# Kernel tuning notes

Measured on AMD Instinct MI355X. Metric: run time of the kernel, lower is better.

The kernel has to match this reference:

```python
import jax, jax.numpy as jnp
import numpy as np

EPS = 1e-6
NEG_SLOPE = 0.2


def setup_inputs() -> dict:
    key = jax.random.key(0)
    k1, k2 = jax.random.split(key)
    B, D, T = 4, 512, 2048
    H, Dh = 8, 512 // 8
    x = jax.random.normal(k1, (B, D, T), dtype=jnp.float32)
    qkv = jax.random.normal(k2, (3, H, D, Dh), dtype=jnp.float32) * 0.02
    norm_w = jnp.ones((1,), dtype=jnp.float32)
    return {"x": x, "qkv": qkv, "norm_w": norm_w}


def reference(x, qkv, norm_w):
    B, D, T = x.shape
    H = qkv.shape[1]
    # leaky relu on channels-first input
    x = jnp.where(x >= 0, x, NEG_SLOPE * x)
    # fused QKV projection: (B,D,T),(3,H,D,Dh) -> (3,B,H,T,Dh)
    h = jnp.einsum('bdt,nhdD->nbhtD', x, qkv)
    # RMSNorm over the sequence axis (dim=-2), scalar learned weight
    denom = jnp.mean(h * h, axis=-2, keepdims=True)
    h = norm_w * (h / jnp.sqrt(denom + EPS))
    q, k, v = h[0], h[1], h[2]
    scale = jnp.sqrt(jnp.asarray(D // H, dtype=x.dtype))
    # manual attention: (B,H,T,T) score matrix
    attn = jax.nn.softmax(jnp.einsum('bhtD,bhTD->bhtT', q, k) / scale, axis=-1)
    # weighted values, output laid out (B,H,Dh,T) then merged to (B,D,T)
    out = jnp.einsum('bhtT,bhTD->bhDt', attn, v)
    return out.reshape(B, D, T)
```

## Files before the change

### kernel.cpp

```cpp
#include <hip/hip_runtime.h>
#include <cstddef>

#define B   4
#define D   512
#define T   2048
#define H   8
#define DH  64
#define NEG_SLOPE 0.2f
#define EPS 1e-6f
#define LOG2E 1.44269504088896340736f

typedef __attribute__((ext_vector_type(8))) short short8;
typedef __attribute__((ext_vector_type(4))) short sh4;
typedef __attribute__((ext_vector_type(4))) float float4v;

__device__ __forceinline__ float bf2f(ushort u) {
    unsigned int x = ((unsigned int)u) << 16;
    return __builtin_bit_cast(float, x);
}
__device__ __forceinline__ ushort f2bf(float f) {
    unsigned int x = __builtin_bit_cast(unsigned int, f);
    x = x + 0x7fffu + ((x >> 16) & 1u);
    return (ushort)(x >> 16);
}

__global__ __launch_bounds__(256) void transpose_fused(const float* __restrict__ x,
                                                       const float* __restrict__ qkv,
                                                       ushort* __restrict__ xT,
                                                       ushort* __restrict__ WT,
                                                       float* __restrict__ ssq, int zcount) {
    const int tid = threadIdx.x;
    const int z = blockIdx.z;
    if (z == 0 && blockIdx.x == 0 && blockIdx.y == 0) {
        for (int i = tid; i < zcount; i += 256) ssq[i] = 0.f;
    }

    const float* s;
    ushort* d;
    int src_ld, dst_ld, do_lrelu;
    if (z < B) {
        const int c0 = blockIdx.x * 64, r0 = blockIdx.y * 64;
        s = x + (size_t)z * D * T + (size_t)r0 * T + c0;
        d = xT + (size_t)z * T * D + (size_t)c0 * D + r0;
        src_ld = T; dst_ld = D; do_lrelu = 1;
    } else {
        if (blockIdx.x != 0) return;
        const int g = z - B;
        const int r0 = blockIdx.y * 64;
        s = qkv + (size_t)g * D * DH + (size_t)r0 * DH;
        d = WT + (size_t)g * DH * D + r0;
        src_ld = DH; dst_ld = D; do_lrelu = 0;
    }

    __shared__ float Ls[64][68];
    const int rl = tid >> 4, c4 = (tid & 15) * 4;
    #pragma unroll
    for (int p = 0; p < 4; ++p) {
        float4 v = *(const float4*)(s + (size_t)(rl + p * 16) * src_ld + c4);
        if (do_lrelu) {
            v.x = fmaxf(v.x, NEG_SLOPE * v.x);
            v.y = fmaxf(v.y, NEG_SLOPE * v.y);
            v.z = fmaxf(v.z, NEG_SLOPE * v.z);
            v.w = fmaxf(v.w, NEG_SLOPE * v.w);
        }
        *(float4*)&Ls[rl + p * 16][c4] = v;
    }
    __syncthreads();

    const int tl = tid >> 2;
    #pragma unroll
    for (int it = 0; it < 2; ++it) {
        int ch = (tid & 3) + it * 4;
        ushort o[8];
        #pragma unroll
        for (int j = 0; j < 8; ++j) o[j] = f2bf(Ls[ch * 8 + j][tl]);
        *(uint4*)(d + (size_t)tl * dst_ld + ch * 8) = *(uint4*)o;
    }
}

__global__ __launch_bounds__(256) void qkv_mm(const ushort* __restrict__ xT,
                                              const ushort* __restrict__ WT,
                                              ushort* __restrict__ hb,
                                              ushort* __restrict__ vT,
                                              float* __restrict__ ssq) {
    const int tid = threadIdx.x, wave = tid >> 6, lane = tid & 63;
    const int quad = lane >> 4, l16 = lane & 15;
    const int wr = wave >> 1, wc = wave & 1;
    const int t0  = blockIdx.x * 128;
    const int gd0 = blockIdx.y * 128;
    const int b   = blockIdx.z;

    __shared__ ushort SMEM[2 * 128 * 64];
    ushort* At = SMEM;
    ushort* Bt = SMEM + 128 * 64;

    const ushort* xb = xT + (size_t)b * T * D + (size_t)t0 * D;
    const ushort* wb = WT + (size_t)gd0 * D;

    const int srow = lane >> 3;
    const int csrc = (lane & 7) ^ srow;
    const bool is_v = (blockIdx.y >= 8);
    const ushort* Asrc = is_v ? At : Bt;
    const ushort* Bsrc = is_v ? Bt : At;
    const int arow0 = is_v ? wr * 64 : wc * 64;
    const int brow0 = is_v ? wc * 64 : wr * 64;

    float4v acc[4][4];
    #pragma unroll
    for (int i = 0; i < 4; ++i)
        #pragma unroll
        for (int j = 0; j < 4; ++j) acc[i][j] = (float4v){0.f, 0.f, 0.f, 0.f};

    for (int k0 = 0; k0 < D; k0 += 64) {
        #pragma unroll
        for (int i = 0; i < 4; ++i) {
            int rbase = wave * 32 + i * 8;
            int row = rbase + srow;
            __builtin_amdgcn_global_load_lds(
                (const __attribute__((address_space(1))) unsigned int*)(xb + (size_t)row * D + k0 + csrc * 8),
                (__attribute__((address_space(3))) unsigned int*)&At[rbase * 64], 16, 0, 0);
            __builtin_amdgcn_global_load_lds(
                (const __attribute__((address_space(1))) unsigned int*)(wb + (size_t)row * D + k0 + csrc * 8),
                (__attribute__((address_space(3))) unsigned int*)&Bt[rbase * 64], 16, 0, 0);
        }
        __syncthreads();

        #pragma unroll
        for (int kh = 0; kh < 2; ++kh) {
            short8 aF[4], bF[4];
            #pragma unroll
            for (int mt = 0; mt < 4; ++mt) {
                int row = arow0 + mt * 16 + l16;
                aF[mt] = *(const short8*)&Asrc[row * 64 + (((kh * 4 + quad) ^ (l16 & 7)) * 8)];
            }
            #pragma unroll
            for (int nt = 0; nt < 4; ++nt) {
                int row = brow0 + nt * 16 + l16;
                bF[nt] = *(const short8*)&Bsrc[row * 64 + (((kh * 4 + quad) ^ (l16 & 7)) * 8)];
            }
            #pragma unroll
            for (int mt = 0; mt < 4; ++mt)
                #pragma unroll
                for (int nt = 0; nt < 4; ++nt)
                    acc[mt][nt] = __builtin_amdgcn_mfma_f32_16x16x32_bf16(
                        aF[mt], bF[nt], acc[mt][nt], 0, 0, 0);
        }
        __syncthreads();
    }

    const int g  = blockIdx.y * 2 + wc;
    const int n  = g >> 3, hh = g & 7;
    const int ch = ((n * B + b) * H + hh) * 64;
    ushort* E = SMEM + wave * 4096;

    #pragma unroll
    for (int mt = 0; mt < 4; ++mt) {
        #pragma unroll
        for (int nt = 0; nt < 4; ++nt) {
            float4v c = acc[mt][nt];
            ushort4 pk;
            pk.x = f2bf(c[0]); pk.y = f2bf(c[1]);
            pk.z = f2bf(c[2]); pk.w = f2bf(c[3]);
            int row   = nt * 16 + l16;
            int chunk = mt * 2 + (quad >> 1);
            int pos   = chunk ^ (l16 & 7);
            *(ushort4*)&E[row * 64 + pos * 8 + (quad & 1) * 4] = pk;
        }
    }

    const int rsub = lane >> 3;
    const int csub = lane & 7;
    const int posr = csub ^ rsub;

    if (!is_v) {
        ushort* hbase = hb + (((size_t)n * B + b) * H + hh) * (size_t)T * DH
                        + (size_t)(t0 + wr * 64) * DH;
        float sq8[8] = {0.f, 0.f, 0.f, 0.f, 0.f, 0.f, 0.f, 0.f};
        #pragma unroll
        for (int i = 0; i < 8; ++i) {
            uint4 v = *(const uint4*)&E[(i * 8 + rsub) * 64 + posr * 8];
            const ushort* u = (const ushort*)&v;
            #pragma unroll
            for (int j = 0; j < 8; ++j) { float f = bf2f(u[j]); sq8[j] += f * f; }
            *(uint4*)(hbase + (size_t)(i * 8 + rsub) * DH + csub * 8) = v;
        }
        #pragma unroll
        for (int j = 0; j < 8; ++j) {
            float s = sq8[j];
            s += __shfl_xor(s, 8); s += __shfl_xor(s, 16); s += __shfl_xor(s, 32);
            if (lane < 8) atomicAdd(&ssq[ch + lane * 8 + j], s);
        }
    } else {
        ushort* vbase = vT + ((size_t)b * H + hh) * (size_t)DH * T + (t0 + wr * 64);
        #pragma unroll
        for (int i = 0; i < 8; ++i) {
            uint4 v = *(const uint4*)&E[(i * 8 + rsub) * 64 + posr * 8];
            const ushort* u = (const ushort*)&v;
            float s = 0.f;
            #pragma unroll
            for (int j = 0; j < 8; ++j) { float f = bf2f(u[j]); s += f * f; }
            *(uint4*)(vbase + (size_t)(i * 8 + rsub) * T + csub * 8) = v;
            s += __shfl_xor(s, 1); s += __shfl_xor(s, 2); s += __shfl_xor(s, 4);
            if ((lane & 7) == 0) atomicAdd(&ssq[ch + i * 8 + rsub], s);
        }
    }
}

__global__ __launch_bounds__(256) void flash_attn(const ushort* __restrict__ hb,
                                                  const ushort* __restrict__ vT,
                                                  const float* __restrict__ ssq,
                                                  const float* __restrict__ norm_w,
                                                  float* __restrict__ out) {
    const int tid  = threadIdx.x;
    const int wave = tid >> 6;
    const int lane = tid & 63;
    const int quad = lane >> 4;
    const int l16  = lane & 15;

    const int lin  = blockIdx.x;
    const int head = ((lin & 7) << 2) | ((lin >> 3) & 3);
    const int t0   = (lin >> 5) * 128;
    const int b    = head >> 3, hh = head & 7;

    const size_t slab = (size_t)B * H * T * DH;
    const ushort* qp = hb + (size_t)head * T * DH;
    const ushort* kp = hb + slab + (size_t)head * T * DH;
    const ushort* vp = vT + (size_t)head * DH * T;

    __shared__ ushort Kt[2][64 * 64];
    __shared__ ushort Vt[2][64 * 64];
    __shared__ float fqk[64], sv[64];

    if (tid < 64) {
        float nw = norm_w[0];
        float mq = ssq[(0 * B * H + head) * 64 + tid] * (1.0f / T) + EPS;
        float mk = ssq[(1 * B * H + head) * 64 + tid] * (1.0f / T) + EPS;
        float mv = ssq[(2 * B * H + head) * 64 + tid] * (1.0f / T) + EPS;
        fqk[tid] = nw * nw * rsqrtf(mq) * rsqrtf(mk) * 0.125f * LOG2E;
        sv[tid]  = nw * rsqrtf(mv);
    }
    __syncthreads();

    short8 bQ[2][2];
    #pragma unroll
    for (int qg = 0; qg < 2; ++qg) {
        const ushort* qr = qp + (size_t)(t0 + wave * 32 + qg * 16 + l16) * DH;
        #pragma unroll
        for (int kh = 0; kh < 2; ++kh) {
            short8 raw = *(const short8*)(qr + kh * 32 + quad * 8);
            #pragma unroll
            for (int j = 0; j < 8; ++j) {
                float f = bf2f((ushort)raw[j]) * fqk[kh * 32 + quad * 8 + j];
                bQ[qg][kh][j] = (short)f2bf(f);
            }
        }
    }

    const int srow = lane >> 3;
    const int csrc = (lane & 7) ^ srow;
    const ushort* kA = kp + (size_t)(wave * 16 + srow) * DH + csrc * 8;
    const ushort* kB = kp + (size_t)(wave * 16 + 8 + srow) * DH + csrc * 8;
    const ushort* vA = vp + (size_t)(wave * 16 + srow) * T + csrc * 8;
    const ushort* vB = vp + (size_t)(wave * 16 + 8 + srow) * T + csrc * 8;

    float l_run[2] = {0.f, 0.f};
    float4v O[2][4];
    #pragma unroll
    for (int qg = 0; qg < 2; ++qg)
        #pragma unroll
        for (int dt = 0; dt < 4; ++dt) O[qg][dt] = (float4v){0.f, 0.f, 0.f, 0.f};

    __builtin_amdgcn_global_load_lds(
        (const __attribute__((address_space(1))) unsigned int*)kA,
        (__attribute__((address_space(3))) unsigned int*)&Kt[0][(wave * 16) * 64], 16, 0, 0);
    __builtin_amdgcn_global_load_lds(
        (const __attribute__((address_space(1))) unsigned int*)kB,
        (__attribute__((address_space(3))) unsigned int*)&Kt[0][(wave * 16 + 8) * 64], 16, 0, 0);
    __builtin_amdgcn_global_load_lds(
        (const __attribute__((address_space(1))) unsigned int*)vA,
        (__attribute__((address_space(3))) unsigned int*)&Vt[0][(wave * 16) * 64], 16, 0, 0);
    __builtin_amdgcn_global_load_lds(
        (const __attribute__((address_space(1))) unsigned int*)vB,
        (__attribute__((address_space(3))) unsigned int*)&Vt[0][(wave * 16 + 8) * 64], 16, 0, 0);

    for (int jt = 0; jt < 32; ++jt) {
        __syncthreads();
        if (jt < 31) {
            const int pn = (jt + 1) & 1;
            const size_t jk = (size_t)(jt + 1) * 64;
            __builtin_amdgcn_global_load_lds(
                (const __attribute__((address_space(1))) unsigned int*)(kA + jk * DH),
                (__attribute__((address_space(3))) unsigned int*)&Kt[pn][(wave * 16) * 64], 16, 0, 0);
            __builtin_amdgcn_global_load_lds(
                (const __attribute__((address_space(1))) unsigned int*)(kB + jk * DH),
                (__attribute__((address_space(3))) unsigned int*)&Kt[pn][(wave * 16 + 8) * 64], 16, 0, 0);
            __builtin_amdgcn_global_load_lds(
                (const __attribute__((address_space(1))) unsigned int*)(vA + jk),
                (__attribute__((address_space(3))) unsigned int*)&Vt[pn][(wave * 16) * 64], 16, 0, 0);
            __builtin_amdgcn_global_load_lds(
                (const __attribute__((address_space(1))) unsigned int*)(vB + jk),
                (__attribute__((address_space(3))) unsigned int*)&Vt[pn][(wave * 16 + 8) * 64], 16, 0, 0);
        }
        const int p = jt & 1;

        float4v S[2][4];
        #pragma unroll
        for (int qg = 0; qg < 2; ++qg)
            #pragma unroll
            for (int mt = 0; mt < 4; ++mt) S[qg][mt] = (float4v){0.f, 0.f, 0.f, 0.f};
        #pragma unroll
        for (int kh = 0; kh < 2; ++kh) {
            #pragma unroll
            for (int mt = 0; mt < 4; ++mt) {
                int row = mt * 16 + l16;
                short8 aK = *(const short8*)&Kt[p][row * 64 + (((kh * 4 + quad) ^ (row & 7)) * 8)];
                #pragma unroll
                for (int qg = 0; qg < 2; ++qg)
                    S[qg][mt] = __builtin_amdgcn_mfma_f32_16x16x32_bf16(aK, bQ[qg][kh], S[qg][mt], 0, 0, 0);
            }
        }

        sh4 bP[2][4];
        #pragma unroll
        for (int qg = 0; qg < 2; ++qg) {
            #pragma unroll
            for (int mt = 0; mt < 4; ++mt) {
                float p0 = __builtin_amdgcn_exp2f(S[qg][mt][0]);
                float p1 = __builtin_amdgcn_exp2f(S[qg][mt][1]);
                float p2 = __builtin_amdgcn_exp2f(S[qg][mt][2]);
                float p3 = __builtin_amdgcn_exp2f(S[qg][mt][3]);
                l_run[qg] += (p0 + p1) + (p2 + p3);
                unsigned int a0 = __builtin_bit_cast(unsigned int, p0) + 0x8000u;
                unsigned int a1 = __builtin_bit_cast(unsigned int, p1) + 0x8000u;
                unsigned int a2 = __builtin_bit_cast(unsigned int, p2) + 0x8000u;
                unsigned int a3 = __builtin_bit_cast(unsigned int, p3) + 0x8000u;
                uint2 pk;
                pk.x = __builtin_amdgcn_perm(a1, a0, 0x07060302u);
                pk.y = __builtin_amdgcn_perm(a3, a2, 0x07060302u);
                bP[qg][mt] = __builtin_bit_cast(sh4, pk);
            }
        }

        #pragma unroll
        for (int mt = 0; mt < 4; ++mt) {
            #pragma unroll
            for (int dt = 0; dt < 4; ++dt) {
                int dd = dt * 16 + l16;
                sh4 aV = *(const sh4*)&Vt[p][dd * 64 + (((mt * 2 + (quad >> 1)) ^ (dd & 7)) * 8)
                                            + (quad & 1) * 4];
                #pragma unroll
                for (int qg = 0; qg < 2; ++qg)
                    O[qg][dt] = __builtin_amdgcn_mfma_f32_16x16x16bf16_1k(
                        aV, bP[qg][mt], O[qg][dt], 0, 0, 0);
            }
        }
    }

    #pragma unroll
    for (int qg = 0; qg < 2; ++qg) {
        float rs = l_run[qg];
        rs += __shfl_xor(rs, 16);
        rs += __shfl_xor(rs, 32);
        float inv = 1.f / rs;
        const int t = t0 + wave * 32 + qg * 16 + l16;
        #pragma unroll
        for (int dt = 0; dt < 4; ++dt) {
            #pragma unroll
            for (int r = 0; r < 4; ++r) {
                int dd = dt * 16 + quad * 4 + r;
                out[((size_t)b * D + hh * DH + dd) * T + t] = O[qg][dt][r] * inv * sv[dd];
            }
        }
    }
}

extern "C" void kernel_launch(void* const* d_in, const int* in_sizes, int n_in,
                              void* d_out, int out_size, void* d_ws, size_t ws_size,
                              hipStream_t stream) {
    const float* x      = (const float*)d_in[0];
    const float* qkv    = (const float*)d_in[1];
    const float* norm_w = (const float*)d_in[2];
    float* out = (float*)d_out;

    const size_t HB_BYTES = (size_t)2 * B * H * T * DH * 2;
    const size_t VT_BYTES = (size_t)B * H * DH * T * 2;
    const size_t XT_BYTES = (size_t)B * T * D * 2;
    const size_t WT_BYTES = (size_t)3 * H * DH * D * 2;
    ushort* hb  = (ushort*)d_ws;
    ushort* vT  = (ushort*)((char*)d_ws + HB_BYTES);
    ushort* xT  = (ushort*)((char*)d_ws + HB_BYTES + VT_BYTES);
    ushort* WT  = (ushort*)((char*)d_ws + HB_BYTES + VT_BYTES + XT_BYTES);
    float*  ssq = (float*)((char*)d_ws + HB_BYTES + VT_BYTES + XT_BYTES + WT_BYTES);
    const int SSQ_N = 3 * B * H * DH;

    transpose_fused<<<dim3(T / 64, D / 64, B + 3 * H), 256, 0, stream>>>(
        x, qkv, xT, WT, ssq, SSQ_N);
    qkv_mm<<<dim3(T / 128, (3 * H * DH) / 128, B), 256, 0, stream>>>(xT, WT, hb, vT, ssq);
    flash_attn<<<dim3((T / 128) * B * H), 256, 0, stream>>>(hb, vT, ssq, norm_w, out);
}
```

Measured before the change: 164.0 us.

## Use single-wave attention blocks with waitcnt-interleaved K/V prefetch

The attention kernel now runs one 64-thread wave per block covering 32 query rows, so the grid is four times larger. Each wave loads the whole K and V tiles into single-buffered LDS on its own. K and V loads for the next tile are issued right after their last use and guarded with explicit vmcnt waits instead of __syncthreads and double buffering. This removes block-wide barriers and shrinks LDS per block, which should allow more resident blocks. The cost is that K/V tiles are no longer shared across four waves, roughly quadrupling L2/global traffic for K and V, and the overlap depends on the hand-placed waitcnt values.

```diff
diff --git a/kernel.cpp b/kernel.cpp
--- a/kernel.cpp
+++ b/kernel.cpp
@@ -13,6 +13,9 @@
 typedef __attribute__((ext_vector_type(8))) short short8;
 typedef __attribute__((ext_vector_type(4))) short sh4;
 typedef __attribute__((ext_vector_type(4))) float float4v;
+
+#define WAIT_VM8() __builtin_amdgcn_s_waitcnt(0x0F78)
+#define WAIT_VM0() __builtin_amdgcn_s_waitcnt(0x0F70)
 
 __device__ __forceinline__ float bf2f(ushort u) {
     unsigned int x = ((unsigned int)u) << 16;
@@ -206,20 +209,18 @@
     }
 }
 
-__global__ __launch_bounds__(256) void flash_attn(const ushort* __restrict__ hb,
-                                                  const ushort* __restrict__ vT,
-                                                  const float* __restrict__ ssq,
-                                                  const float* __restrict__ norm_w,
-                                                  float* __restrict__ out) {
-    const int tid  = threadIdx.x;
-    const int wave = tid >> 6;
-    const int lane = tid & 63;
+__global__ __launch_bounds__(64) void flash_attn(const ushort* __restrict__ hb,
+                                                 const ushort* __restrict__ vT,
+                                                 const float* __restrict__ ssq,
+                                                 const float* __restrict__ norm_w,
+                                                 float* __restrict__ out) {
+    const int lane = threadIdx.x;
     const int quad = lane >> 4;
     const int l16  = lane & 15;
 
     const int lin  = blockIdx.x;
     const int head = ((lin & 7) << 2) | ((lin >> 3) & 3);
-    const int t0   = (lin >> 5) * 128;
+    const int t0   = (lin >> 5) * 32;
     const int b    = head >> 3, hh = head & 7;
 
     const size_t slab = (size_t)B * H * T * DH;
@@ -227,24 +228,24 @@
     const ushort* kp = hb + slab + (size_t)head * T * DH;
     const ushort* vp = vT + (size_t)head * DH * T;
 
-    __shared__ ushort Kt[2][64 * 64];
-    __shared__ ushort Vt[2][64 * 64];
+    __shared__ ushort Kt[64 * 64];
+    __shared__ ushort Vt[64 * 64];
     __shared__ float fqk[64], sv[64];
 
-    if (tid < 64) {
+    {
         float nw = norm_w[0];
-        float mq = ssq[(0 * B * H + head) * 64 + tid] * (1.0f / T) + EPS;
-        float mk = ssq[(1 * B * H + head) * 64 + tid] * (1.0f / T) + EPS;
-        float mv = ssq[(2 * B * H + head) * 64 + tid] * (1.0f / T) + EPS;
-        fqk[tid] = nw * nw * rsqrtf(mq) * rsqrtf(mk) * 0.125f * LOG2E;
-        sv[tid]  = nw * rsqrtf(mv);
+        float mq = ssq[(0 * B * H + head) * 64 + lane] * (1.0f / T) + EPS;
+        float mk = ssq[(1 * B * H + head) * 64 + lane] * (1.0f / T) + EPS;
+        float mv = ssq[(2 * B * H + head) * 64 + lane] * (1.0f / T) + EPS;
+        fqk[lane] = nw * nw * rsqrtf(mq) * rsqrtf(mk) * 0.125f * LOG2E;
+        sv[lane]  = nw * rsqrtf(mv);
     }
     __syncthreads();
 
     short8 bQ[2][2];
     #pragma unroll
     for (int qg = 0; qg < 2; ++qg) {
-        const ushort* qr = qp + (size_t)(t0 + wave * 32 + qg * 16 + l16) * DH;
+        const ushort* qr = qp + (size_t)(t0 + qg * 16 + l16) * DH;
         #pragma unroll
         for (int kh = 0; kh < 2; ++kh) {
             short8 raw = *(const short8*)(qr + kh * 32 + quad * 8);
@@ -258,10 +259,8 @@
 
     const int srow = lane >> 3;
     const int csrc = (lane & 7) ^ srow;
-    const ushort* kA = kp + (size_t)(wave * 16 + srow) * DH + csrc * 8;
-    const ushort* kB = kp + (size_t)(wave * 16 + 8 + srow) * DH + csrc * 8;
-    const ushort* vA = vp + (size_t)(wave * 16 + srow) * T + csrc * 8;
-    const ushort* vB = vp + (size_t)(wave * 16 + 8 + srow) * T + csrc * 8;
+    const ushort* kS = kp + (size_t)srow * DH + csrc * 8;
+    const ushort* vS = vp + (size_t)srow * T + csrc * 8;
 
     float l_run[2] = {0.f, 0.f};
     float4v O[2][4];
@@ -270,90 +269,94 @@
         #pragma unroll
         for (int dt = 0; dt < 4; ++dt) O[qg][dt] = (float4v){0.f, 0.f, 0.f, 0.f};
 
-    __builtin_amdgcn_global_load_lds(
-        (const __attribute__((address_space(1))) unsigned int*)kA,
-        (__attribute__((address_space(3))) unsigned int*)&Kt[0][(wave * 16) * 64], 16, 0, 0);
-    __builtin_amdgcn_global_load_lds(
-        (const __attribute__((address_space(1))) unsigned int*)kB,
-        (__attribute__((address_space(3))) unsigned int*)&Kt[0][(wave * 16 + 8) * 64], 16, 0, 0);
-    __builtin_amdgcn_global_load_lds(
-        (const __attribute__((address_space(1))) unsigned int*)vA,
-        (__attribute__((address_space(3))) unsigned int*)&Vt[0][(wave * 16) * 64], 16, 0, 0);
-    __builtin_amdgcn_global_load_lds(
-        (const __attribute__((address_space(1))) unsigned int*)vB,
-        (__attribute__((address_space(3))) unsigned int*)&Vt[0][(wave * 16 + 8) * 64], 16, 0, 0);
-
-    for (int jt = 0; jt < 32; ++jt) {
-        __syncthreads();
-        if (jt < 31) {
-            const int pn = (jt + 1) & 1;
-            const size_t jk = (size_t)(jt + 1) * 64;
-            __builtin_amdgcn_global_load_lds(
-                (const __attribute__((address_space(1))) unsigned int*)(kA + jk * DH),
-                (__attribute__((address_space(3))) unsigned int*)&Kt[pn][(wave * 16) * 64], 16, 0, 0);
-            __builtin_amdgcn_global_load_lds(
-                (const __attribute__((address_space(1))) unsigned int*)(kB + jk * DH),
-                (__attribute__((address_space(3))) unsigned int*)&Kt[pn][(wave * 16 + 8) * 64], 16, 0, 0);
-            __builtin_amdgcn_global_load_lds(
-                (const __attribute__((address_space(1))) unsigned int*)(vA + jk),
-                (__attribute__((address_space(3))) unsigned int*)&Vt[pn][(wave * 16) * 64], 16, 0, 0);
-            __builtin_amdgcn_global_load_lds(
-                (const __attribute__((address_space(1))) unsigned int*)(vB + jk),
-                (__attribute__((address_space(3))) unsigned int*)&Vt[pn][(wave * 16 + 8) * 64], 16, 0, 0);
-        }
-        const int p = jt & 1;
-
+    #define ISSUE_K(JT)                                                              \
+        _Pragma("unroll")                                                            \
+        for (int i = 0; i < 8; ++i)                                                  \
+            __builtin_amdgcn_global_load_lds(                                        \
+                (const __attribute__((address_space(1))) unsigned int*)              \
+                    (kS + (size_t)((JT) * 64 + i * 8) * DH),                         \
+                (__attribute__((address_space(3))) unsigned int*)&Kt[i * 512], 16, 0, 0);
+    #define ISSUE_V(JT)                                                              \
+        _Pragma("unroll")                                                            \
+        for (int i = 0; i < 8; ++i)                                                  \
+            __builtin_amdgcn_global_load_lds(                                        \
+                (const __attribute__((address_space(1))) unsigned int*)              \
+                    (vS + (size_t)(i * 8) * T + (JT) * 64),                          \
+                (__attribute__((address_space(3))) unsigned int*)&Vt[i * 512], 16, 0, 0);
+
+    #define DO_QK(Sv)                                                                \
+        _Pragma("unroll")                                                            \
+        for (int qg = 0; qg < 2; ++qg)                                               \
+            _Pragma("unroll")                                                        \
+            for (int mt = 0; mt < 4; ++mt) Sv[qg][mt] = (float4v){0.f,0.f,0.f,0.f};  \
+        _Pragma("unroll")                                                            \
+        for (int kh = 0; kh < 2; ++kh) {                                             \
+            _Pragma("unroll")                                                        \
+            for (int mt = 0; mt < 4; ++mt) {                                         \
+                int row = mt * 16 + l16;                                             \
+                short8 aK = *(const short8*)&Kt[row * 64 + (((kh * 4 + quad) ^ (row & 7)) * 8)]; \
+                _Pragma("unroll")                                                    \
+                for (int qg = 0; qg < 2; ++qg)                                       \
+                    Sv[qg][mt] = __builtin_amdgcn_mfma_f32_16x16x32_bf16(aK, bQ[qg][kh], Sv[qg][mt], 0, 0, 0); \
+            }                                                                        \
+        }
+
+    #define DO_EXP(Sv, bPv)                                                          \
+        _Pragma("unroll")                                                            \
+        for (int qg = 0; qg < 2; ++qg) {                                             \
+            _Pragma("unroll")                                                        \
+            for (int mt = 0; mt < 4; ++mt) {                                         \
+                float p0 = __builtin_amdgcn_exp2f(Sv[qg][mt][0]);                    \
+                float p1 = __builtin_amdgcn_exp2f(Sv[qg][mt][1]);                    \
+                float p2 = __builtin_amdgcn_exp2f(Sv[qg][mt][2]);                    \
+                float p3 = __builtin_amdgcn_exp2f(Sv[qg][mt][3]);                    \
+                l_run[qg] += (p0 + p1) + (p2 + p3);                                  \
+                unsigned int a0 = __builtin_bit_cast(unsigned int, p0) + 0x8000u;    \
+                unsigned int a1 = __builtin_bit_cast(unsigned int, p1) + 0x8000u;    \
+                unsigned int a2 = __builtin_bit_cast(unsigned int, p2) + 0x8000u;    \
+                unsigned int a3 = __builtin_bit_cast(unsigned int, p3) + 0x8000u;    \
+                uint2 pk;                                                            \
+                pk.x = __builtin_amdgcn_perm(a1, a0, 0x07060302u);                   \
+                pk.y = __builtin_amdgcn_perm(a3, a2, 0x07060302u);                   \
+                bPv[qg][mt] = __builtin_bit_cast(sh4, pk);                           \
+            }                                                                        \
+        }
+
+    #define DO_PV(bPv)                                                               \
+        _Pragma("unroll")                                                            \
+        for (int mt = 0; mt < 4; ++mt) {                                             \
+            _Pragma("unroll")                                                        \
+            for (int dt = 0; dt < 4; ++dt) {                                         \
+                int dd = dt * 16 + l16;                                              \
+                sh4 aV = *(const sh4*)&Vt[dd * 64 + (((mt * 2 + (quad >> 1)) ^ (dd & 7)) * 8) + (quad & 1) * 4]; \
+                _Pragma("unroll")                                                    \
+                for (int qg = 0; qg < 2; ++qg)                                       \
+                    O[qg][dt] = __builtin_amdgcn_mfma_f32_16x16x16bf16_1k(aV, bPv[qg][mt], O[qg][dt], 0, 0, 0); \
+            }                                                                        \
+        }
+
+    ISSUE_K(0);
+    ISSUE_V(0);
+    WAIT_VM8();
+
+    for (int jt = 0; jt < 31; ++jt) {
         float4v S[2][4];
-        #pragma unroll
-        for (int qg = 0; qg < 2; ++qg)
-            #pragma unroll
-            for (int mt = 0; mt < 4; ++mt) S[qg][mt] = (float4v){0.f, 0.f, 0.f, 0.f};
-        #pragma unroll
-        for (int kh = 0; kh < 2; ++kh) {
-            #pragma unroll
-            for (int mt = 0; mt < 4; ++mt) {
-                int row = mt * 16 + l16;
-                short8 aK = *(const short8*)&Kt[p][row * 64 + (((kh * 4 + quad) ^ (row & 7)) * 8)];
-                #pragma unroll
-                for (int qg = 0; qg < 2; ++qg)
-                    S[qg][mt] = __builtin_amdgcn_mfma_f32_16x16x32_bf16(aK, bQ[qg][kh], S[qg][mt], 0, 0, 0);
-            }
-        }
-
         sh4 bP[2][4];
-        #pragma unroll
-        for (int qg = 0; qg < 2; ++qg) {
-            #pragma unroll
-            for (int mt = 0; mt < 4; ++mt) {
-                float p0 = __builtin_amdgcn_exp2f(S[qg][mt][0]);
-                float p1 = __builtin_amdgcn_exp2f(S[qg][mt][1]);
-                float p2 = __builtin_amdgcn_exp2f(S[qg][mt][2]);
-                float p3 = __builtin_amdgcn_exp2f(S[qg][mt][3]);
-                l_run[qg] += (p0 + p1) + (p2 + p3);
-                unsigned int a0 = __builtin_bit_cast(unsigned int, p0) + 0x8000u;
-                unsigned int a1 = __builtin_bit_cast(unsigned int, p1) + 0x8000u;
-                unsigned int a2 = __builtin_bit_cast(unsigned int, p2) + 0x8000u;
-                unsigned int a3 = __builtin_bit_cast(unsigned int, p3) + 0x8000u;
-                uint2 pk;
-                pk.x = __builtin_amdgcn_perm(a1, a0, 0x07060302u);
-                pk.y = __builtin_amdgcn_perm(a3, a2, 0x07060302u);
-                bP[qg][mt] = __builtin_bit_cast(sh4, pk);
-            }
-        }
-
-        #pragma unroll
-        for (int mt = 0; mt < 4; ++mt) {
-            #pragma unroll
-            for (int dt = 0; dt < 4; ++dt) {
-                int dd = dt * 16 + l16;
-                sh4 aV = *(const sh4*)&Vt[p][dd * 64 + (((mt * 2 + (quad >> 1)) ^ (dd & 7)) * 8)
-                                            + (quad & 1) * 4];
-                #pragma unroll
-                for (int qg = 0; qg < 2; ++qg)
-                    O[qg][dt] = __builtin_amdgcn_mfma_f32_16x16x16bf16_1k(
-                        aV, bP[qg][mt], O[qg][dt], 0, 0, 0);
-            }
-        }
+        DO_QK(S);
+        ISSUE_K(jt + 1);
+        DO_EXP(S, bP);
+        WAIT_VM8();
+        DO_PV(bP);
+        ISSUE_V(jt + 1);
+        WAIT_VM8();
+    }
+    {
+        float4v S[2][4];
+        sh4 bP[2][4];
+        DO_QK(S);
+        DO_EXP(S, bP);
+        WAIT_VM0();
+        DO_PV(bP);
     }
 
     #pragma unroll
@@ -362,7 +365,7 @@
         rs += __shfl_xor(rs, 16);
         rs += __shfl_xor(rs, 32);
         float inv = 1.f / rs;
-        const int t = t0 + wave * 32 + qg * 16 + l16;
+        const int t = t0 + qg * 16 + l16;
         #pragma unroll
         for (int dt = 0; dt < 4; ++dt) {
             #pragma unroll
@@ -396,5 +399,5 @@
     transpose_fused<<<dim3(T / 64, D / 64, B + 3 * H), 256, 0, stream>>>(
         x, qkv, xT, WT, ssq, SSQ_N);
     qkv_mm<<<dim3(T / 128, (3 * H * DH) / 128, B), 256, 0, stream>>>(xT, WT, hb, vT, ssq);
-    flash_attn<<<dim3((T / 128) * B * H), 256, 0, stream>>>(hb, vT, ssq, norm_w, out);
-}
+    flash_attn<<<dim3((T / 32) * B * H), 64, 0, stream>>>(hb, vT, ssq, norm_w, out);
+}
```

Result: slower. 188.6 us (+15.0%).
